# Kernel optimization log

Hardware: AMD Instinct MI355X
Metric: run time of the kernel (lower is better)

Reference implementation:

```python
import jax, jax.numpy as jnp
import numpy as np

N_NODES = 50000
N_EDGES = 1600000
NODE_DIM = 64
HID = 16


def setup_inputs() -> dict:
    key = jax.random.key(0)
    ks = jax.random.split(key, 12)
    f = lambda k, shape: (jax.random.normal(k, shape, dtype=jnp.float32) * 0.1)
    edge_index = jax.random.randint(ks[0], (2, N_EDGES), 0, N_NODES)
    return {
        "edge_index": edge_index,
        "node_emb": f(ks[1], (N_NODES, NODE_DIM)),
        "edge_emb": f(ks[2], (N_EDGES, HID)),
        "W1": f(ks[3], (NODE_DIM, HID)),
        "att_src1": f(ks[4], (HID,)),
        "att_dst1": f(ks[5], (HID,)),
        "b1": jnp.zeros((HID,), jnp.float32),
        "W2": f(ks[6], (HID, HID)),
        "att_src2": f(ks[7], (HID,)),
        "att_dst2": f(ks[8], (HID,)),
        "b2": jnp.zeros((HID,), jnp.float32),
        "Wm1": f(ks[9], (3 * HID, HID)),
        "bm1": jnp.zeros((HID,), jnp.float32),
        "Wm2": f(ks[10], (HID, 1)),
        "bm2": jnp.zeros((1,), jnp.float32),
    }


def gat_layer(x, src, dst, W, a_src, a_dst, b, num_nodes):
    # Single-head GATConv (PyG defaults): self-loops, leaky_relu(0.2), softmax over dst.
    h = x @ W  # [N, out]
    logits = jax.nn.leaky_relu((h @ a_src)[src] + (h @ a_dst)[dst], negative_slope=0.2)
    m = jax.ops.segment_max(logits, dst, num_segments=num_nodes)  # stable softmax
    e = jnp.exp(logits - jax.lax.stop_gradient(m)[dst])
    denom = jax.ops.segment_sum(e, dst, num_segments=num_nodes)
    coef = e / denom[dst]  # [E+N]
    out = jax.ops.segment_sum(coef[:, None] * h[src], dst, num_segments=num_nodes)
    return out + b


def reference(edge_index, node_emb, edge_emb, W1, att_src1, att_dst1, b1,
              W2, att_src2, att_dst2, b2, Wm1, bm1, Wm2, bm2):
    src, dst = edge_index[0], edge_index[1]
    num_nodes = node_emb.shape[0]
    loops = jnp.arange(num_nodes)
    src_f = jnp.concatenate([src, loops])  # GATConv add_self_loops=True
    dst_f = jnp.concatenate([dst, loops])

    x = node_emb
    for (W, a_s, a_d, b) in [(W1, att_src1, att_dst1, b1), (W2, att_src2, att_dst2, b2)]:
        x = gat_layer(x, src_f, dst_f, W, a_s, a_d, b, num_nodes)
        x = jax.nn.gelu(x, approximate=False)  # torch F.gelu default = exact erf
        # dropout omitted (eval mode)

    # Vectorized replacement of the per-edge Python loop:
    edge_repr = jnp.concatenate([x[src], x[dst], edge_emb], axis=1)  # [E, 3*HID]
    hmid = jax.nn.relu(edge_repr @ Wm1 + bm1)
    probs = jax.nn.sigmoid(hmid @ Wm2 + bm2)[:, 0]  # [E]
    return probs
```

## Files before the change

### kernel.cpp

```cpp
#include <hip/hip_runtime.h>
#include <math.h>

#define N_NODES 50000
#define N_EDGES 1600000
#define NODE_DIM 64
#define HID 16
#define BSZ 64
#define NBUCK ((N_NODES + BSZ - 1) / BSZ)
#define CAPB 2560
#define EPB 8192
#define APB 256
#define APPEND_BLOCKS ((N_EDGES + EPB - 1) / EPB)

typedef _Float16 h8 __attribute__((ext_vector_type(8)));

__global__ void append_kernel(const int* __restrict__ ei,
                              int* __restrict__ gcount,
                              unsigned int* __restrict__ blist) {
    __shared__ int lcount[NBUCK];
    __shared__ int gbase[NBUCK];
    __shared__ int loff[NBUCK];
    int t = threadIdx.x;
    for (int b = t; b < NBUCK; b += APB) { lcount[b] = 0; loff[b] = 0; }
    __syncthreads();
    long base = (long)blockIdx.x * EPB;
#pragma unroll
    for (int k = 0; k < EPB / APB; k++) {
        long i = base + k * APB + t;
        if (i < N_EDGES) atomicAdd(&lcount[ei[N_EDGES + i] >> 6], 1);
    }
    __syncthreads();
    for (int b = t; b < NBUCK; b += APB) {
        int c = lcount[b];
        gbase[b] = c ? atomicAdd(&gcount[b], c) : 0;
    }
    __syncthreads();
#pragma unroll
    for (int k = 0; k < EPB / APB; k++) {
        long i = base + k * APB + t;
        if (i < N_EDGES) {
            int s = ei[i], d = ei[N_EDGES + i];
            int b = d >> 6;
            int pos = gbase[b] + atomicAdd(&loff[b], 1);
            if (pos < CAPB)
                blist[(size_t)b * CAPB + pos] = ((unsigned)(d & 63) << 16) | (unsigned)s;
        }
    }
}

__global__ void sort_kernel(const int* __restrict__ gcount, const unsigned int* __restrict__ blist,
                            unsigned short* __restrict__ csr, int* __restrict__ dstbeg) {
    __shared__ int cnts[BSZ];
    __shared__ int sc[BSZ];
    __shared__ int off[BSZ];
    int b = blockIdx.x, t = threadIdx.x;
    if (t < BSZ) cnts[t] = 0;
    __syncthreads();
    int cnt = gcount[b]; if (cnt > CAPB) cnt = CAPB;
    const unsigned int* lp = blist + (size_t)b * CAPB;
    for (int k = t; k < cnt; k += APB) atomicAdd(&cnts[lp[k] >> 16], 1);
    __syncthreads();
    if (t < BSZ) sc[t] = cnts[t];
    __syncthreads();
    for (int o = 1; o < BSZ; o <<= 1) {
        int v = 0;
        if (t < BSZ && t >= o) v = sc[t - o];
        __syncthreads();
        if (t < BSZ) sc[t] += v;
        __syncthreads();
    }
    if (t < BSZ) {
        int beg = sc[t] - cnts[t];
        off[t] = beg;
        dstbeg[(b << 6) + t] = beg;
    }
    __syncthreads();
    for (int k = t; k < cnt; k += APB) {
        unsigned int r = lp[k];
        int pos = atomicAdd(&off[r >> 16], 1);
        csr[(size_t)b * CAPB + pos] = (unsigned short)(r & 0xFFFF);
    }
}

__global__ void node_h64(const float* __restrict__ x,
                         const float* __restrict__ W,
                         const float* __restrict__ a_src,
                         const float* __restrict__ a_dst,
                         float* __restrict__ h,
                         float* __restrict__ as_, float* __restrict__ ad_) {
    __shared__ float Ws[NODE_DIM * HID];
    __shared__ float asv[HID], adv[HID];
    int t = threadIdx.x;
    for (int i = t; i < NODE_DIM * HID; i += blockDim.x) Ws[i] = W[i];
    if (t < HID) { asv[t] = a_src[t]; adv[t] = a_dst[t]; }
    __syncthreads();
    int n = blockIdx.x * blockDim.x + t;
    if (n >= N_NODES) return;
    float acc[HID];
#pragma unroll
    for (int j = 0; j < HID; j++) acc[j] = 0.f;
    const float4* xr = (const float4*)(x + (size_t)n * NODE_DIM);
#pragma unroll
    for (int k4 = 0; k4 < NODE_DIM / 4; k4++) {
        float4 xv = xr[k4];
        const float* w0 = Ws + (k4 * 4) * HID;
#pragma unroll
        for (int j = 0; j < HID; j++)
            acc[j] += xv.x * w0[j] + xv.y * w0[HID + j] + xv.z * w0[2 * HID + j] + xv.w * w0[3 * HID + j];
    }
    float s = 0.f, d = 0.f;
#pragma unroll
    for (int j = 0; j < HID; j++) {
        h[(size_t)n * HID + j] = acc[j];
        s += acc[j] * asv[j];
        d += acc[j] * adv[j];
    }
    as_[n] = s; ad_[n] = d;
}

__global__ void node_h16(const float* __restrict__ x,
                         const float* __restrict__ W,
                         const float* __restrict__ a_src,
                         const float* __restrict__ a_dst,
                         float* __restrict__ h,
                         float* __restrict__ as_, float* __restrict__ ad_) {
    __shared__ float Ws[HID * HID];
    __shared__ float asv[HID], adv[HID];
    int t = threadIdx.x;
    for (int i = t; i < HID * HID; i += blockDim.x) Ws[i] = W[i];
    if (t < HID) { asv[t] = a_src[t]; adv[t] = a_dst[t]; }
    __syncthreads();
    int n = blockIdx.x * blockDim.x + t;
    if (n >= N_NODES) return;
    float acc[HID];
#pragma unroll
    for (int j = 0; j < HID; j++) acc[j] = 0.f;
    const float* xr = x + (size_t)n * HID;
#pragma unroll
    for (int k = 0; k < HID; k++) {
        float xv = xr[k];
#pragma unroll
        for (int j = 0; j < HID; j++) acc[j] += xv * Ws[k * HID + j];
    }
    float s = 0.f, d = 0.f;
#pragma unroll
    for (int j = 0; j < HID; j++) {
        h[(size_t)n * HID + j] = acc[j];
        s += acc[j] * asv[j];
        d += acc[j] * adv[j];
    }
    as_[n] = s; ad_[n] = d;
}

__global__ void gather_kernel(const int* __restrict__ gcount, const int* __restrict__ dstbeg,
                              const unsigned short* __restrict__ csr,
                              const float* __restrict__ h,
                              const float* __restrict__ as_, const float* __restrict__ ad_,
                              const float* __restrict__ b,
                              float* __restrict__ xout) {
    int g = blockIdx.x * (blockDim.x >> 4) + (threadIdx.x >> 4);
    int j = threadIdx.x & 15;
    if (g >= N_NODES) return;
    int bk = g >> 6, dl = g & 63;
    int cnt_b = gcount[bk]; if (cnt_b > CAPB) cnt_b = CAPB;
    int beg = dstbeg[g];
    int end = (dl < 63) ? dstbeg[g + 1] : cnt_b;
    if (end > cnt_b) end = cnt_b;
    if (beg > end) beg = end;
    const unsigned short* row = csr + (size_t)bk * CAPB + beg;
    int cnt = end - beg;
    float adn = ad_[g];
    float acc = 0.f, den = 0.f;
    int k = 0;
    for (; k + 4 <= cnt; k += 4) {
        int s0 = row[k], s1 = row[k + 1], s2 = row[k + 2], s3 = row[k + 3];
        float l0 = as_[s0] + adn, l1 = as_[s1] + adn;
        float l2 = as_[s2] + adn, l3 = as_[s3] + adn;
        l0 = l0 > 0.f ? l0 : 0.2f * l0;
        l1 = l1 > 0.f ? l1 : 0.2f * l1;
        l2 = l2 > 0.f ? l2 : 0.2f * l2;
        l3 = l3 > 0.f ? l3 : 0.2f * l3;
        float e0 = expf(l0), e1 = expf(l1), e2 = expf(l2), e3 = expf(l3);
        float h0 = h[(size_t)s0 * HID + j], h1 = h[(size_t)s1 * HID + j];
        float h2 = h[(size_t)s2 * HID + j], h3 = h[(size_t)s3 * HID + j];
        den += (e0 + e1) + (e2 + e3);
        acc += (e0 * h0 + e1 * h1) + (e2 * h2 + e3 * h3);
    }
    for (; k < cnt; k++) {
        int s = row[k];
        float lg = as_[s] + adn;
        lg = lg > 0.f ? lg : 0.2f * lg;
        float e = expf(lg);
        den += e;
        acc += e * h[(size_t)s * HID + j];
    }
    float lg = as_[g] + adn;
    lg = lg > 0.f ? lg : 0.2f * lg;
    float e = expf(lg);
    den += e;
    acc += e * h[(size_t)g * HID + j];
    float v = acc / den + b[j];
    xout[(size_t)g * HID + j] = 0.5f * v * (1.f + erff(v * 0.70710678118654752f));
}

__global__ void edge_prep(const float* __restrict__ x,
                          const float* __restrict__ Wm1,
                          const float* __restrict__ bm1,
                          _Float16* __restrict__ A,
                          _Float16* __restrict__ B) {
    __shared__ float Wa[HID * HID];
    __shared__ float Wb[HID * HID];
    __shared__ float bs[HID];
    int t = threadIdx.x;
    for (int i = t; i < HID * HID; i += blockDim.x) {
        Wa[i] = Wm1[i];
        Wb[i] = Wm1[HID * HID + i];
    }
    if (t < HID) bs[t] = bm1[t];
    __syncthreads();
    int n = blockIdx.x * blockDim.x + t;
    if (n >= N_NODES) return;
    float xr[HID];
    const float4* xp = (const float4*)(x + (size_t)n * HID);
#pragma unroll
    for (int q = 0; q < 4; q++) {
        float4 v = xp[q];
        xr[4 * q] = v.x; xr[4 * q + 1] = v.y; xr[4 * q + 2] = v.z; xr[4 * q + 3] = v.w;
    }
    float a[HID], bb[HID];
#pragma unroll
    for (int j = 0; j < HID; j++) { a[j] = bs[j]; bb[j] = 0.f; }
#pragma unroll
    for (int k = 0; k < HID; k++) {
        float xv = xr[k];
#pragma unroll
        for (int j = 0; j < HID; j++) {
            a[j]  += xv * Wa[k * HID + j];
            bb[j] += xv * Wb[k * HID + j];
        }
    }
    h8 a0, a1, b0, b1;
#pragma unroll
    for (int j = 0; j < 8; j++) {
        a0[j] = (_Float16)a[j];      a1[j] = (_Float16)a[8 + j];
        b0[j] = (_Float16)bb[j];     b1[j] = (_Float16)bb[8 + j];
    }
    h8* Ap = (h8*)(A + (size_t)n * HID);
    h8* Bp = (h8*)(B + (size_t)n * HID);
    Ap[0] = a0; Ap[1] = a1;
    Bp[0] = b0; Bp[1] = b1;
}

__global__ void edge_mlp(const int* __restrict__ ei,
                         const _Float16* __restrict__ A,
                         const _Float16* __restrict__ B,
                         const float* __restrict__ ee,
                         const float* __restrict__ Wm1,
                         const float* __restrict__ Wm2,
                         const float* __restrict__ bm2,
                         float* __restrict__ out) {
    __shared__ float We[HID * HID];
    __shared__ float W2s[HID];
    __shared__ float b2s;
    int t = threadIdx.x;
    for (int i = t; i < HID * HID; i += blockDim.x) We[i] = Wm1[2 * HID * HID + i];
    if (t < HID) W2s[t] = Wm2[t];
    if (t == 0) b2s = bm2[0];
    __syncthreads();
    long i = (long)blockIdx.x * blockDim.x + t;
    if (i >= N_EDGES) return;
    int s = ei[i], d = ei[N_EDGES + i];
    const h8* Ap = (const h8*)(A + (size_t)s * HID);
    const h8* Bp = (const h8*)(B + (size_t)d * HID);
    h8 a0 = Ap[0], a1 = Ap[1];
    h8 b0 = Bp[0], b1 = Bp[1];
    const float4* ep = (const float4*)(ee + (size_t)i * HID);
    float4 e0 = ep[0], e1 = ep[1], e2 = ep[2], e3 = ep[3];
    float a[HID];
#pragma unroll
    for (int j = 0; j < 8; j++) {
        a[j]     = (float)a0[j] + (float)b0[j];
        a[8 + j] = (float)a1[j] + (float)b1[j];
    }
    float ev[HID];
    ev[0]  = e0.x; ev[1]  = e0.y; ev[2]  = e0.z; ev[3]  = e0.w;
    ev[4]  = e1.x; ev[5]  = e1.y; ev[6]  = e1.z; ev[7]  = e1.w;
    ev[8]  = e2.x; ev[9]  = e2.y; ev[10] = e2.z; ev[11] = e2.w;
    ev[12] = e3.x; ev[13] = e3.y; ev[14] = e3.z; ev[15] = e3.w;
    const float4* W4 = (const float4*)We;
#pragma unroll
    for (int k = 0; k < HID; k++) {
        float e1v = ev[k];
        float4 w0 = W4[k * 4 + 0], w1 = W4[k * 4 + 1], w2 = W4[k * 4 + 2], w3 = W4[k * 4 + 3];
        a[0]  += e1v * w0.x; a[1]  += e1v * w0.y; a[2]  += e1v * w0.z; a[3]  += e1v * w0.w;
        a[4]  += e1v * w1.x; a[5]  += e1v * w1.y; a[6]  += e1v * w1.z; a[7]  += e1v * w1.w;
        a[8]  += e1v * w2.x; a[9]  += e1v * w2.y; a[10] += e1v * w2.z; a[11] += e1v * w2.w;
        a[12] += e1v * w3.x; a[13] += e1v * w3.y; a[14] += e1v * w3.z; a[15] += e1v * w3.w;
    }
    float o = b2s;
#pragma unroll
    for (int j = 0; j < HID; j++) o += fmaxf(a[j], 0.f) * W2s[j];
    out[i] = 1.f / (1.f + expf(-o));
}

extern "C" void kernel_launch(void* const* d_in, const int* in_sizes, int n_in,
                              void* d_out, int out_size, void* d_ws, size_t ws_size,
                              hipStream_t stream) {
    const int*   ei       = (const int*)d_in[0];
    const float* node_emb = (const float*)d_in[1];
    const float* edge_emb = (const float*)d_in[2];
    const float* W1       = (const float*)d_in[3];
    const float* att_src1 = (const float*)d_in[4];
    const float* att_dst1 = (const float*)d_in[5];
    const float* b1       = (const float*)d_in[6];
    const float* W2       = (const float*)d_in[7];
    const float* att_src2 = (const float*)d_in[8];
    const float* att_dst2 = (const float*)d_in[9];
    const float* b2       = (const float*)d_in[10];
    const float* Wm1      = (const float*)d_in[11];
    const float* bm1      = (const float*)d_in[12];
    const float* Wm2      = (const float*)d_in[13];
    const float* bm2      = (const float*)d_in[14];
    float* out            = (float*)d_out;

    char* w = (char*)d_ws;
    float*          h      = (float*)w;          w += (size_t)N_NODES * HID * 4;
    float*          xcur   = (float*)w;          w += (size_t)N_NODES * HID * 4;
    float*          as_    = (float*)w;          w += (size_t)N_NODES * 4;
    float*          ad_    = (float*)w;          w += (size_t)N_NODES * 4;
    int*            gcount = (int*)w;            w += (size_t)NBUCK * 4;
    unsigned int*   blist  = (unsigned int*)w;   w += (size_t)NBUCK * CAPB * 4;
    unsigned short* csr    = (unsigned short*)w; w += (size_t)NBUCK * CAPB * 2;
    int*            dstbeg = (int*)w;            w += (size_t)NBUCK * BSZ * 4;

    _Float16* Anode = (_Float16*)blist;
    _Float16* Bnode = Anode + (size_t)N_NODES * HID;

    const int BT = 256;
    int nblk_node = (N_NODES + BT - 1) / BT;
    int nblk_E    = (N_EDGES + BT - 1) / BT;
    int nblk_g    = (N_NODES * HID + BT - 1) / BT;

    hipMemsetAsync(gcount, 0, (size_t)NBUCK * sizeof(int), stream);
    append_kernel<<<APPEND_BLOCKS, APB, 0, stream>>>(ei, gcount, blist);
    sort_kernel<<<NBUCK, APB, 0, stream>>>(gcount, blist, csr, dstbeg);

    node_h64<<<nblk_node, BT, 0, stream>>>(node_emb, W1, att_src1, att_dst1, h, as_, ad_);
    gather_kernel<<<nblk_g, BT, 0, stream>>>(gcount, dstbeg, csr, h, as_, ad_, b1, xcur);

    node_h16<<<nblk_node, BT, 0, stream>>>(xcur, W2, att_src2, att_dst2, h, as_, ad_);
    gather_kernel<<<nblk_g, BT, 0, stream>>>(gcount, dstbeg, csr, h, as_, ad_, b2, xcur);

    edge_prep<<<nblk_node, BT, 0, stream>>>(xcur, Wm1, bm1, Anode, Bnode);
    edge_mlp<<<nblk_E, BT, 0, stream>>>(ei, Anode, Bnode, edge_emb, Wm1, Wm2, bm2, out);
}
```

Before: 353.3 us.

## Fuse per-node transforms into gather epilogues and shrink append block size

The layer-2 node transform (h = x@W2 plus attention scalars) moves into the first gather's epilogue, and the edge-MLP per-node projections (A, B) move into the second gather's epilogue. Both use 16-lane shuffles to broadcast the node vector, which removes two kernel launches and the round trips of the intermediate x through global memory. New buffers for h2/as2/ad2 are placed in the free tail of the blist region. Separately, edges per append block drop from 8192 to 2048, giving more blocks for the bucket append at the cost of more global atomics.

```diff
diff --git a/kernel.cpp b/kernel.cpp
--- a/kernel.cpp
+++ b/kernel.cpp
@@ -8,7 +8,7 @@
 #define BSZ 64
 #define NBUCK ((N_NODES + BSZ - 1) / BSZ)
 #define CAPB 2560
-#define EPB 8192
+#define EPB 2048
 #define APB 256
 #define APPEND_BLOCKS ((N_EDGES + EPB - 1) / EPB)
 
@@ -118,48 +118,28 @@
     as_[n] = s; ad_[n] = d;
 }
 
-__global__ void node_h16(const float* __restrict__ x,
-                         const float* __restrict__ W,
-                         const float* __restrict__ a_src,
-                         const float* __restrict__ a_dst,
-                         float* __restrict__ h,
-                         float* __restrict__ as_, float* __restrict__ ad_) {
-    __shared__ float Ws[HID * HID];
-    __shared__ float asv[HID], adv[HID];
-    int t = threadIdx.x;
-    for (int i = t; i < HID * HID; i += blockDim.x) Ws[i] = W[i];
-    if (t < HID) { asv[t] = a_src[t]; adv[t] = a_dst[t]; }
-    __syncthreads();
-    int n = blockIdx.x * blockDim.x + t;
-    if (n >= N_NODES) return;
-    float acc[HID];
-#pragma unroll
-    for (int j = 0; j < HID; j++) acc[j] = 0.f;
-    const float* xr = x + (size_t)n * HID;
-#pragma unroll
-    for (int k = 0; k < HID; k++) {
-        float xv = xr[k];
-#pragma unroll
-        for (int j = 0; j < HID; j++) acc[j] += xv * Ws[k * HID + j];
-    }
-    float s = 0.f, d = 0.f;
-#pragma unroll
-    for (int j = 0; j < HID; j++) {
-        h[(size_t)n * HID + j] = acc[j];
-        s += acc[j] * asv[j];
-        d += acc[j] * adv[j];
-    }
-    as_[n] = s; ad_[n] = d;
-}
-
-__global__ void gather_kernel(const int* __restrict__ gcount, const int* __restrict__ dstbeg,
+__global__ void gather1_fused(const int* __restrict__ gcount, const int* __restrict__ dstbeg,
                               const unsigned short* __restrict__ csr,
                               const float* __restrict__ h,
                               const float* __restrict__ as_, const float* __restrict__ ad_,
                               const float* __restrict__ b,
-                              float* __restrict__ xout) {
-    int g = blockIdx.x * (blockDim.x >> 4) + (threadIdx.x >> 4);
-    int j = threadIdx.x & 15;
+                              const float* __restrict__ W2,
+                              const float* __restrict__ a_src2,
+                              const float* __restrict__ a_dst2,
+                              float* __restrict__ h2out,
+                              float* __restrict__ as2, float* __restrict__ ad2) {
+    __shared__ float Ws[HID * HID];
+    __shared__ float asv[HID], adv[HID], bs[HID];
+    int t = threadIdx.x;
+    for (int i = t; i < HID * HID; i += blockDim.x) Ws[i] = W2[i];
+    if (t < HID) { asv[t] = a_src2[t]; adv[t] = a_dst2[t]; bs[t] = b[t]; }
+    __syncthreads();
+    int j = t & 15;
+    float Wcol[HID];
+#pragma unroll
+    for (int k = 0; k < HID; k++) Wcol[k] = Ws[k * HID + j];
+    float a2j = asv[j], d2j = adv[j], bj = bs[j];
+    int g = blockIdx.x * (blockDim.x >> 4) + (t >> 4);
     if (g >= N_NODES) return;
     int bk = g >> 6, dl = g & 63;
     int cnt_b = gcount[bk]; if (cnt_b > CAPB) cnt_b = CAPB;
@@ -199,56 +179,98 @@
     float e = expf(lg);
     den += e;
     acc += e * h[(size_t)g * HID + j];
-    float v = acc / den + b[j];
-    xout[(size_t)g * HID + j] = 0.5f * v * (1.f + erff(v * 0.70710678118654752f));
-}
-
-__global__ void edge_prep(const float* __restrict__ x,
-                          const float* __restrict__ Wm1,
-                          const float* __restrict__ bm1,
-                          _Float16* __restrict__ A,
-                          _Float16* __restrict__ B) {
+    float v = acc / den + bj;
+    v = 0.5f * v * (1.f + erff(v * 0.70710678118654752f));
+    float acc2 = 0.f;
+#pragma unroll
+    for (int k2 = 0; k2 < HID; k2++) {
+        float xk = __shfl(v, k2, 16);
+        acc2 += xk * Wcol[k2];
+    }
+    h2out[(size_t)g * HID + j] = acc2;
+    float ps = acc2 * a2j, pd = acc2 * d2j;
+#pragma unroll
+    for (int o = 1; o < 16; o <<= 1) {
+        ps += __shfl_xor(ps, o, 16);
+        pd += __shfl_xor(pd, o, 16);
+    }
+    if (j == 0) { as2[g] = ps; ad2[g] = pd; }
+}
+
+__global__ void gather2_fused(const int* __restrict__ gcount, const int* __restrict__ dstbeg,
+                              const unsigned short* __restrict__ csr,
+                              const float* __restrict__ h,
+                              const float* __restrict__ as_, const float* __restrict__ ad_,
+                              const float* __restrict__ b,
+                              const float* __restrict__ Wm1,
+                              const float* __restrict__ bm1,
+                              _Float16* __restrict__ A, _Float16* __restrict__ B) {
     __shared__ float Wa[HID * HID];
     __shared__ float Wb[HID * HID];
-    __shared__ float bs[HID];
+    __shared__ float bs[HID], b1s[HID];
     int t = threadIdx.x;
     for (int i = t; i < HID * HID; i += blockDim.x) {
         Wa[i] = Wm1[i];
         Wb[i] = Wm1[HID * HID + i];
     }
-    if (t < HID) bs[t] = bm1[t];
-    __syncthreads();
-    int n = blockIdx.x * blockDim.x + t;
-    if (n >= N_NODES) return;
-    float xr[HID];
-    const float4* xp = (const float4*)(x + (size_t)n * HID);
-#pragma unroll
-    for (int q = 0; q < 4; q++) {
-        float4 v = xp[q];
-        xr[4 * q] = v.x; xr[4 * q + 1] = v.y; xr[4 * q + 2] = v.z; xr[4 * q + 3] = v.w;
-    }
-    float a[HID], bb[HID];
-#pragma unroll
-    for (int j = 0; j < HID; j++) { a[j] = bs[j]; bb[j] = 0.f; }
-#pragma unroll
-    for (int k = 0; k < HID; k++) {
-        float xv = xr[k];
-#pragma unroll
-        for (int j = 0; j < HID; j++) {
-            a[j]  += xv * Wa[k * HID + j];
-            bb[j] += xv * Wb[k * HID + j];
-        }
-    }
-    h8 a0, a1, b0, b1;
-#pragma unroll
-    for (int j = 0; j < 8; j++) {
-        a0[j] = (_Float16)a[j];      a1[j] = (_Float16)a[8 + j];
-        b0[j] = (_Float16)bb[j];     b1[j] = (_Float16)bb[8 + j];
-    }
-    h8* Ap = (h8*)(A + (size_t)n * HID);
-    h8* Bp = (h8*)(B + (size_t)n * HID);
-    Ap[0] = a0; Ap[1] = a1;
-    Bp[0] = b0; Bp[1] = b1;
+    if (t < HID) { bs[t] = b[t]; b1s[t] = bm1[t]; }
+    __syncthreads();
+    int j = t & 15;
+    float WaC[HID], WbC[HID];
+#pragma unroll
+    for (int k = 0; k < HID; k++) { WaC[k] = Wa[k * HID + j]; WbC[k] = Wb[k * HID + j]; }
+    float bj = bs[j], b1j = b1s[j];
+    int g = blockIdx.x * (blockDim.x >> 4) + (t >> 4);
+    if (g >= N_NODES) return;
+    int bk = g >> 6, dl = g & 63;
+    int cnt_b = gcount[bk]; if (cnt_b > CAPB) cnt_b = CAPB;
+    int beg = dstbeg[g];
+    int end = (dl < 63) ? dstbeg[g + 1] : cnt_b;
+    if (end > cnt_b) end = cnt_b;
+    if (beg > end) beg = end;
+    const unsigned short* row = csr + (size_t)bk * CAPB + beg;
+    int cnt = end - beg;
+    float adn = ad_[g];
+    float acc = 0.f, den = 0.f;
+    int k = 0;
+    for (; k + 4 <= cnt; k += 4) {
+        int s0 = row[k], s1 = row[k + 1], s2 = row[k + 2], s3 = row[k + 3];
+        float l0 = as_[s0] + adn, l1 = as_[s1] + adn;
+        float l2 = as_[s2] + adn, l3 = as_[s3] + adn;
+        l0 = l0 > 0.f ? l0 : 0.2f * l0;
+        l1 = l1 > 0.f ? l1 : 0.2f * l1;
+        l2 = l2 > 0.f ? l2 : 0.2f * l2;
+        l3 = l3 > 0.f ? l3 : 0.2f * l3;
+        float e0 = expf(l0), e1 = expf(l1), e2 = expf(l2), e3 = expf(l3);
+        float h0 = h[(size_t)s0 * HID + j], h1 = h[(size_t)s1 * HID + j];
+        float h2 = h[(size_t)s2 * HID + j], h3 = h[(size_t)s3 * HID + j];
+        den += (e0 + e1) + (e2 + e3);
+        acc += (e0 * h0 + e1 * h1) + (e2 * h2 + e3 * h3);
+    }
+    for (; k < cnt; k++) {
+        int s = row[k];
+        float lg = as_[s] + adn;
+        lg = lg > 0.f ? lg : 0.2f * lg;
+        float e = expf(lg);
+        den += e;
+        acc += e * h[(size_t)s * HID + j];
+    }
+    float lg = as_[g] + adn;
+    lg = lg > 0.f ? lg : 0.2f * lg;
+    float e = expf(lg);
+    den += e;
+    acc += e * h[(size_t)g * HID + j];
+    float v = acc / den + bj;
+    v = 0.5f * v * (1.f + erff(v * 0.70710678118654752f));
+    float accA = b1j, accB = 0.f;
+#pragma unroll
+    for (int k2 = 0; k2 < HID; k2++) {
+        float xk = __shfl(v, k2, 16);
+        accA += xk * WaC[k2];
+        accB += xk * WbC[k2];
+    }
+    A[(size_t)g * HID + j] = (_Float16)accA;
+    B[(size_t)g * HID + j] = (_Float16)accB;
 }
 
 __global__ void edge_mlp(const int* __restrict__ ei,
@@ -325,7 +347,7 @@
 
     char* w = (char*)d_ws;
     float*          h      = (float*)w;          w += (size_t)N_NODES * HID * 4;
-    float*          xcur   = (float*)w;          w += (size_t)N_NODES * HID * 4;
+    float*          h2     = (float*)w;          w += (size_t)N_NODES * HID * 4;
     float*          as_    = (float*)w;          w += (size_t)N_NODES * 4;
     float*          ad_    = (float*)w;          w += (size_t)N_NODES * 4;
     int*            gcount = (int*)w;            w += (size_t)NBUCK * 4;
@@ -335,6 +357,8 @@
 
     _Float16* Anode = (_Float16*)blist;
     _Float16* Bnode = Anode + (size_t)N_NODES * HID;
+    float*    as2   = (float*)(Bnode + (size_t)N_NODES * HID);
+    float*    ad2   = as2 + N_NODES;
 
     const int BT = 256;
     int nblk_node = (N_NODES + BT - 1) / BT;
@@ -346,11 +370,11 @@
     sort_kernel<<<NBUCK, APB, 0, stream>>>(gcount, blist, csr, dstbeg);
 
     node_h64<<<nblk_node, BT, 0, stream>>>(node_emb, W1, att_src1, att_dst1, h, as_, ad_);
-    gather_kernel<<<nblk_g, BT, 0, stream>>>(gcount, dstbeg, csr, h, as_, ad_, b1, xcur);
-
-    node_h16<<<nblk_node, BT, 0, stream>>>(xcur, W2, att_src2, att_dst2, h, as_, ad_);
-    gather_kernel<<<nblk_g, BT, 0, stream>>>(gcount, dstbeg, csr, h, as_, ad_, b2, xcur);
-
-    edge_prep<<<nblk_node, BT, 0, stream>>>(xcur, Wm1, bm1, Anode, Bnode);
+    gather1_fused<<<nblk_g, BT, 0, stream>>>(gcount, dstbeg, csr, h, as_, ad_, b1,
+                                             W2, att_src2, att_dst2, h2, as2, ad2);
+
+    gather2_fused<<<nblk_g, BT, 0, stream>>>(gcount, dstbeg, csr, h2, as2, ad2, b2,
+                                             Wm1, bm1, Anode, Bnode);
+
     edge_mlp<<<nblk_E, BT, 0, stream>>>(ei, Anode, Bnode, edge_emb, Wm1, Wm2, bm2, out);
 }
```

After: 346.9 us. No clear change (-1.8%).
